# Kernel tuning notes

Measured on AMD Instinct MI355X. Metric: run time of the kernel, lower is better.

Reference implementation:

```python
import jax, jax.numpy as jnp
import numpy as np

B, K, H, W, N = 256, 16, 64, 64, 1024   # batch, channels (n_ch), grid H/W, sampled sites
F_IN = 9 * K - 1                         # 3x3 neighborhood * K channels, minus center channel


def setup_inputs() -> dict:
    key = jax.random.key(0)
    ks = jax.random.split(key, 8)
    z_int = jax.random.randint(ks[0], (B, K, H, W), 0, 16, dtype=jnp.int32)
    bs = jax.random.randint(ks[1], (N,), 0, K, dtype=jnp.int32)
    ii = jax.random.randint(ks[2], (N,), 0, H, dtype=jnp.int32)
    jj = jax.random.randint(ks[3], (N,), 0, W, dtype=jnp.int32)
    W1 = jax.random.normal(ks[4], (F_IN, 128), dtype=jnp.float32) * 0.05
    b1 = jnp.zeros((128,), dtype=jnp.float32)
    W2 = jax.random.normal(ks[5], (128, 16), dtype=jnp.float32) * 0.05
    b2 = jnp.zeros((16,), dtype=jnp.float32)
    return {"z_int": z_int, "bs": bs, "ii": ii, "jj": jj,
            "W1": W1, "b1": b1, "W2": W2, "b2": b2}


def _gather_ctx(z_f, bs, ii, jj):
    # Faithful to get_context ordering: loops di, dj (each in [-1,0,1]) then b,
    # skipping (di==0, dj==0, b==bi). Flattened skip position = 4*K + bi.
    off = jnp.array([-1, 0, 1], dtype=jnp.int32)
    di = jnp.repeat(off, 3)          # [9]
    dj = jnp.tile(off, 3)            # [9]
    ni = (ii[:, None] + di[None, :]) % H   # [N, 9] toroidal wrap
    nj = (jj[:, None] + dj[None, :]) % W   # [N, 9]
    ctx = z_f[:, :, ni, nj]                # [B, K, N, 9]
    ctx = jnp.transpose(ctx, (2, 0, 3, 1)).reshape(N, B, 9 * K)  # [N, B, 9K], (di,dj) major then b
    drop = 4 * K + bs                      # [N] center-channel flat index
    idx = jnp.arange(F_IN, dtype=jnp.int32)
    keep = idx[None, :] + (idx[None, :] >= drop[:, None]).astype(jnp.int32)  # [N, F_IN]
    return jax.vmap(lambda c, k: c[:, k])(ctx, keep)  # [N, B, F_IN]


def reference(z_int, bs, ii, jj, W1, b1, W2, b2):
    z_f = z_int.astype(jnp.float32) / 15.0
    ctx = _gather_ctx(z_f, bs, ii, jj)                 # [N, B, 9K-1]
    h = jax.nn.relu(jnp.einsum('nbf,fh->nbh', ctx, W1) + b1)
    logits = jnp.einsum('nbh,hc->nbc', h, W2) + b2     # [N, B, 16]
    pred = jnp.argmax(logits, axis=-1)                 # [N, B]
    tgt = z_int[:, bs, ii, jj].T                       # [N, B]
    rate = jnp.mean((pred != tgt).astype(jnp.float32)) # np.mean of per-site mean == global mean
    return rate
```

## Files before the change

kernel.cpp:

```cpp
#include <hip/hip_runtime.h>
#include <stdint.h>

#define NB 1024
#define BB 256
#define KK 16
#define HH 64
#define WW 64
#define F_FULL 144
#define HDIM 128
#define CDIM 16
#define KPAD 160
#define APITCH 168
#define HPITCH 136
#define ABYTES (64 * APITCH * 2)
#define HBYTES (64 * HPITCH * 2)
#define NCTR 128

typedef __bf16 bf16x8 __attribute__((ext_vector_type(8)));
typedef float f32x4 __attribute__((ext_vector_type(4)));

#define W1T_OFF 1024
#define W1T_BYTES (16 * HDIM * KPAD * 2)
#define W2B_OFF (W1T_OFF + W1T_BYTES)
#define W2B_BYTES (CDIM * HDIM * 2)
#define ZT_OFF (W2B_OFF + W2B_BYTES)

__device__ __forceinline__ unsigned short bf16_bits(float v) {
    __bf16 b = (__bf16)v;
    return __builtin_bit_cast(unsigned short, b);
}

#define TP 144
__global__ __launch_bounds__(256) void prep_kernel(
    const int* __restrict__ z, const float* __restrict__ W1,
    const float* __restrict__ W2, uint8_t* __restrict__ zt,
    unsigned short* __restrict__ W1t, unsigned short* __restrict__ W2b,
    int* __restrict__ counters) {
    int bid = blockIdx.x;
    int t = threadIdx.x;
    if (bid < 4096) {
        __shared__ uint8_t tile[32 * TP];
        int bx = bid & 127;
        int by = bid >> 7;
        int c0 = bx * 32, r0 = by * 128;
#pragma unroll
        for (int i = 0; i < 4; ++i) {
            int lin = i * 256 + t;
            int c = lin & 31;
            int rq = lin >> 5;
            uchar4 v;
            v.x = (uint8_t)z[(size_t)(r0 + rq * 4 + 0) * 4096 + c0 + c];
            v.y = (uint8_t)z[(size_t)(r0 + rq * 4 + 1) * 4096 + c0 + c];
            v.z = (uint8_t)z[(size_t)(r0 + rq * 4 + 2) * 4096 + c0 + c];
            v.w = (uint8_t)z[(size_t)(r0 + rq * 4 + 3) * 4096 + c0 + c];
            *(uchar4*)(tile + c * TP + rq * 4) = v;
        }
        __syncthreads();
        int cy = t >> 3, rx = t & 7;
        uint4 v = *(const uint4*)(tile + cy * TP + rx * 16);
        *(uint4*)(zt + (size_t)(c0 + cy) * 4096 + r0 + rx * 16) = v;
    } else if (bid < 5376) {
        int idx = (bid - 4096) * 256 + t;
        int k = idx % KPAD;
        int h = (idx / KPAD) % HDIM;
        int s = idx / (KPAD * HDIM);
        int drop = 4 * KK + s;
        float val = 0.0f;
        if (k < F_FULL && k != drop) {
            int src = k - (k > drop ? 1 : 0);
            val = W1[src * HDIM + h];
        }
        W1t[idx] = bf16_bits(val);
    } else {
        int idx = (bid - 5376) * 256 + t;
        if (idx < CDIM * HDIM) {
            int k = idx % HDIM;
            int c = idx / HDIM;
            W2b[idx] = bf16_bits(W2[k * CDIM + c]);
        }
        if (bid == 5376 && t < NCTR) counters[t] = 0;
    }
}

__global__ __launch_bounds__(256, 2) void main_kernel(
    const uint8_t* __restrict__ zt, const unsigned short* __restrict__ W1t,
    const float* __restrict__ b1, const unsigned short* __restrict__ W2b,
    const float* __restrict__ b2, const int* __restrict__ bs,
    const int* __restrict__ ii, const int* __restrict__ jj,
    int* __restrict__ counters) {
    __shared__ __align__(16) unsigned char smem[2 * ABYTES + HBYTES];
    unsigned short* sA0 = (unsigned short*)smem;
    unsigned short* sA1 = (unsigned short*)(smem + ABYTES);
    unsigned short* sH = (unsigned short*)(smem + 2 * ABYTES);

    int t = threadIdx.x;
    int n = blockIdx.x;
    int wave = t >> 6, lane = t & 63;
    int l15 = lane & 15, l4 = lane >> 4;

    int in_ = ii[n], jn = jj[n], sn = bs[n];

    const unsigned short* w1s = W1t + (size_t)sn * (HDIM * KPAD);
    int n0 = wave * 32;
    bf16x8 Bf[2][5];
#pragma unroll
    for (int nt = 0; nt < 2; ++nt)
#pragma unroll
        for (int ks = 0; ks < 5; ++ks)
            Bf[nt][ks] = *(const bf16x8*)(w1s + (n0 + nt * 16 + l15) * KPAD + ks * 32 + l4 * 8);
    bf16x8 Bf2[4];
#pragma unroll
    for (int ks = 0; ks < 4; ++ks)
        Bf2[ks] = *(const bf16x8*)(W2b + l15 * HDIM + ks * 32 + l4 * 8);
    float b1v0 = b1[n0 + l15], b1v1 = b1[n0 + 16 + l15];
    float b2v = b2[l15];

    if (t < 192) {
        int b = t / 3, part = t % 3;
        *(uint4*)(sA0 + b * APITCH + F_FULL + part * 8) = make_uint4(0, 0, 0, 0);
        *(uint4*)(sA1 + b * APITCH + F_FULL + part * 8) = make_uint4(0, 0, 0, 0);
    }

    uint4 g0, g1, g2;
    auto gload = [&](int tile) {
        int b = (t & 63) + tile * 64;
        int p0 = t >> 6;
        int ni0 = (in_ + p0 / 3 - 1) & (HH - 1);
        int nj0 = (jn + p0 % 3 - 1) & (WW - 1);
        g0 = *(const uint4*)(zt + (((size_t)(ni0 * WW + nj0) * BB + b) << 4));
        int p1 = p0 + 4;
        int ni1 = (in_ + p1 / 3 - 1) & (HH - 1);
        int nj1 = (jn + p1 % 3 - 1) & (WW - 1);
        g1 = *(const uint4*)(zt + (((size_t)(ni1 * WW + nj1) * BB + b) << 4));
        if (t < 64) {
            int ni2 = (in_ + 1) & (HH - 1);
            int nj2 = (jn + 1) & (WW - 1);
            g2 = *(const uint4*)(zt + (((size_t)(ni2 * WW + nj2) * BB + b) << 4));
        }
    };
    auto gwrite = [&](unsigned short* dst) {
        int b = t & 63;
        int p0 = t >> 6;
        auto conv = [&](uint4 raw, int p) {
            const uint8_t* bytes = (const uint8_t*)&raw;
            union { __bf16 h[16]; uint4 q[2]; } u;
#pragma unroll
            for (int k = 0; k < 16; ++k)
                u.h[k] = (__bf16)((float)bytes[k] * (1.0f / 15.0f));
            uint4* d = (uint4*)(dst + b * APITCH + p * 16);
            d[0] = u.q[0];
            d[1] = u.q[1];
        };
        conv(g0, p0);
        conv(g1, p0 + 4);
        if (t < 64) conv(g2, 8);
    };

    gload(0);
    gwrite(sA0);
    int err = 0;
    size_t tbase = ((size_t)(in_ * WW + jn) * BB) << 4;

    for (int tile = 0; tile < 4; ++tile) {
        unsigned short* sA = (tile & 1) ? sA1 : sA0;
        unsigned short* sAnext = (tile & 1) ? sA0 : sA1;

        if (tile < 3) gload(tile + 1);
        __syncthreads();

        int bg0 = tile * 64 + wave * 16 + l4 * 4;
        int tv4[4];
#pragma unroll
        for (int r = 0; r < 4; ++r)
            tv4[r] = zt[tbase + ((size_t)(bg0 + r) << 4) + sn];

        f32x4 acc[4][2] = {};
#pragma unroll
        for (int mt = 0; mt < 4; ++mt) {
            bf16x8 Af[5];
#pragma unroll
            for (int ks = 0; ks < 5; ++ks)
                Af[ks] = *(const bf16x8*)(sA + (mt * 16 + l15) * APITCH + ks * 32 + l4 * 8);
#pragma unroll
            for (int ks = 0; ks < 5; ++ks) {
                acc[mt][0] = __builtin_amdgcn_mfma_f32_16x16x32_bf16(Af[ks], Bf[0][ks], acc[mt][0], 0, 0, 0);
                acc[mt][1] = __builtin_amdgcn_mfma_f32_16x16x32_bf16(Af[ks], Bf[1][ks], acc[mt][1], 0, 0, 0);
            }
        }

#pragma unroll
        for (int mt = 0; mt < 4; ++mt)
#pragma unroll
            for (int nt = 0; nt < 2; ++nt) {
                float bv = nt ? b1v1 : b1v0;
                int hcol = n0 + nt * 16 + l15;
#pragma unroll
                for (int r = 0; r < 4; ++r) {
                    int b = mt * 16 + l4 * 4 + r;
                    float v = fmaxf(acc[mt][nt][r] + bv, 0.0f);
                    sH[b * HPITCH + hcol] = bf16_bits(v);
                }
            }
        __syncthreads();

        f32x4 acc2 = {};
#pragma unroll
        for (int ks = 0; ks < 4; ++ks) {
            bf16x8 Af = *(const bf16x8*)(sH + (wave * 16 + l15) * HPITCH + ks * 32 + l4 * 8);
            acc2 = __builtin_amdgcn_mfma_f32_16x16x32_bf16(Af, Bf2[ks], acc2, 0, 0, 0);
        }

#pragma unroll
        for (int r = 0; r < 4; ++r) {
            float v = acc2[r] + b2v;
            int idx = l15;
#pragma unroll
            for (int m = 1; m < 16; m <<= 1) {
                float ov = __shfl_xor(v, m);
                int oi = __shfl_xor(idx, m);
                if (ov > v || (ov == v && oi < idx)) { v = ov; idx = oi; }
            }
            unsigned long long mm = __ballot(l15 == 0 && idx != tv4[r]);
            err += (int)__popcll(mm);
        }

        if (tile < 3) gwrite(sAnext);
    }

    if (lane == 0) atomicAdd(&counters[n & (NCTR - 1)], err);
}

__global__ void finalize_kernel(const int* __restrict__ counters, float* __restrict__ out) {
    int t = threadIdx.x;
    int s = counters[t] + counters[t + 64];
#pragma unroll
    for (int m = 32; m; m >>= 1) s += __shfl_down(s, m);
    if (t == 0) out[0] = (float)s / (float)(NB * BB);
}

extern "C" void kernel_launch(void* const* d_in, const int* in_sizes, int n_in,
                              void* d_out, int out_size, void* d_ws, size_t ws_size,
                              hipStream_t stream) {
    const int* z = (const int*)d_in[0];
    const int* bs = (const int*)d_in[1];
    const int* ii = (const int*)d_in[2];
    const int* jj = (const int*)d_in[3];
    const float* W1 = (const float*)d_in[4];
    const float* b1 = (const float*)d_in[5];
    const float* W2 = (const float*)d_in[6];
    const float* b2 = (const float*)d_in[7];
    float* out = (float*)d_out;

    uint8_t* ws = (uint8_t*)d_ws;
    int* counters = (int*)ws;
    unsigned short* W1t = (unsigned short*)(ws + W1T_OFF);
    unsigned short* W2b = (unsigned short*)(ws + W2B_OFF);
    uint8_t* zt = ws + ZT_OFF;

    prep_kernel<<<5384, 256, 0, stream>>>(z, W1, W2, zt, W1t, W2b, counters);
    main_kernel<<<NB, 256, 0, stream>>>(zt, W1t, b1, W2b, b2, bs, ii, jj, counters);
    finalize_kernel<<<1, 64, 0, stream>>>(counters, out);
}
```

Baseline: 144.6 us.

## Software-pipeline layer-1 and layer-2 stages with double-buffered hidden tile

Restructures the per-tile loop into a five-stage software pipeline. Layer-2 MFMA and argmax for the previous tile run in the same step as the layer-1 MFMA for the current tile, with the hidden activations double-buffered in shared memory. This drops one __syncthreads per tile, and global loads are now issued two tiles ahead. The cost is extra LDS per block, which may reduce occupancy, and longer register live ranges.

```diff
diff --git a/kernel.cpp b/kernel.cpp
--- a/kernel.cpp
+++ b/kernel.cpp
@@ -88,10 +88,11 @@
     const float* __restrict__ b2, const int* __restrict__ bs,
     const int* __restrict__ ii, const int* __restrict__ jj,
     int* __restrict__ counters) {
-    __shared__ __align__(16) unsigned char smem[2 * ABYTES + HBYTES];
+    __shared__ __align__(16) unsigned char smem[2 * ABYTES + 2 * HBYTES];
     unsigned short* sA0 = (unsigned short*)smem;
     unsigned short* sA1 = (unsigned short*)(smem + ABYTES);
-    unsigned short* sH = (unsigned short*)(smem + 2 * ABYTES);
+    unsigned short* sH0 = (unsigned short*)(smem + 2 * ABYTES);
+    unsigned short* sH1 = (unsigned short*)(smem + 2 * ABYTES + HBYTES);
 
     int t = threadIdx.x;
     int n = blockIdx.x;
@@ -122,9 +123,9 @@
     }
 
     uint4 g0, g1, g2;
+    int p0 = t >> 6;
     auto gload = [&](int tile) {
         int b = (t & 63) + tile * 64;
-        int p0 = t >> 6;
         int ni0 = (in_ + p0 / 3 - 1) & (HH - 1);
         int nj0 = (jn + p0 % 3 - 1) & (WW - 1);
         g0 = *(const uint4*)(zt + (((size_t)(ni0 * WW + nj0) * BB + b) << 4));
@@ -140,7 +141,6 @@
     };
     auto gwrite = [&](unsigned short* dst) {
         int b = t & 63;
-        int p0 = t >> 6;
         auto conv = [&](uint4 raw, int p) {
             const uint8_t* bytes = (const uint8_t*)&raw;
             union { __bf16 h[16]; uint4 q[2]; } u;
@@ -158,73 +158,83 @@
 
     gload(0);
     gwrite(sA0);
+    gload(1);
+
     int err = 0;
     size_t tbase = ((size_t)(in_ * WW + jn) * BB) << 4;
 
-    for (int tile = 0; tile < 4; ++tile) {
-        unsigned short* sA = (tile & 1) ? sA1 : sA0;
-        unsigned short* sAnext = (tile & 1) ? sA0 : sA1;
-
-        if (tile < 3) gload(tile + 1);
+    for (int s = 0; s < 5; ++s) {
         __syncthreads();
 
-        int bg0 = tile * 64 + wave * 16 + l4 * 4;
         int tv4[4];
-#pragma unroll
-        for (int r = 0; r < 4; ++r)
-            tv4[r] = zt[tbase + ((size_t)(bg0 + r) << 4) + sn];
+        if (s >= 1) {
+            int bg0 = (s - 1) * 64 + wave * 16 + l4 * 4;
+#pragma unroll
+            for (int r = 0; r < 4; ++r)
+                tv4[r] = zt[tbase + ((size_t)(bg0 + r) << 4) + sn];
+        }
 
         f32x4 acc[4][2] = {};
-#pragma unroll
-        for (int mt = 0; mt < 4; ++mt) {
-            bf16x8 Af[5];
-#pragma unroll
-            for (int ks = 0; ks < 5; ++ks)
-                Af[ks] = *(const bf16x8*)(sA + (mt * 16 + l15) * APITCH + ks * 32 + l4 * 8);
-#pragma unroll
-            for (int ks = 0; ks < 5; ++ks) {
-                acc[mt][0] = __builtin_amdgcn_mfma_f32_16x16x32_bf16(Af[ks], Bf[0][ks], acc[mt][0], 0, 0, 0);
-                acc[mt][1] = __builtin_amdgcn_mfma_f32_16x16x32_bf16(Af[ks], Bf[1][ks], acc[mt][1], 0, 0, 0);
-            }
-        }
-
-#pragma unroll
-        for (int mt = 0; mt < 4; ++mt)
-#pragma unroll
-            for (int nt = 0; nt < 2; ++nt) {
-                float bv = nt ? b1v1 : b1v0;
-                int hcol = n0 + nt * 16 + l15;
-#pragma unroll
-                for (int r = 0; r < 4; ++r) {
-                    int b = mt * 16 + l4 * 4 + r;
-                    float v = fmaxf(acc[mt][nt][r] + bv, 0.0f);
-                    sH[b * HPITCH + hcol] = bf16_bits(v);
+        if (s < 4) {
+            const unsigned short* sA = (s & 1) ? sA1 : sA0;
+#pragma unroll
+            for (int mt = 0; mt < 4; ++mt) {
+                bf16x8 Af[5];
+#pragma unroll
+                for (int ks = 0; ks < 5; ++ks)
+                    Af[ks] = *(const bf16x8*)(sA + (mt * 16 + l15) * APITCH + ks * 32 + l4 * 8);
+#pragma unroll
+                for (int ks = 0; ks < 5; ++ks) {
+                    acc[mt][0] = __builtin_amdgcn_mfma_f32_16x16x32_bf16(Af[ks], Bf[0][ks], acc[mt][0], 0, 0, 0);
+                    acc[mt][1] = __builtin_amdgcn_mfma_f32_16x16x32_bf16(Af[ks], Bf[1][ks], acc[mt][1], 0, 0, 0);
                 }
             }
-        __syncthreads();
-
-        f32x4 acc2 = {};
-#pragma unroll
-        for (int ks = 0; ks < 4; ++ks) {
-            bf16x8 Af = *(const bf16x8*)(sH + (wave * 16 + l15) * HPITCH + ks * 32 + l4 * 8);
-            acc2 = __builtin_amdgcn_mfma_f32_16x16x32_bf16(Af, Bf2[ks], acc2, 0, 0, 0);
-        }
-
-#pragma unroll
-        for (int r = 0; r < 4; ++r) {
-            float v = acc2[r] + b2v;
-            int idx = l15;
-#pragma unroll
-            for (int m = 1; m < 16; m <<= 1) {
-                float ov = __shfl_xor(v, m);
-                int oi = __shfl_xor(idx, m);
-                if (ov > v || (ov == v && oi < idx)) { v = ov; idx = oi; }
+        }
+
+        if (s >= 1) {
+            const unsigned short* sHp = ((s - 1) & 1) ? sH1 : sH0;
+            f32x4 acc2 = {};
+#pragma unroll
+            for (int ks = 0; ks < 4; ++ks) {
+                bf16x8 Af = *(const bf16x8*)(sHp + (wave * 16 + l15) * HPITCH + ks * 32 + l4 * 8);
+                acc2 = __builtin_amdgcn_mfma_f32_16x16x32_bf16(Af, Bf2[ks], acc2, 0, 0, 0);
             }
-            unsigned long long mm = __ballot(l15 == 0 && idx != tv4[r]);
-            err += (int)__popcll(mm);
-        }
-
-        if (tile < 3) gwrite(sAnext);
+#pragma unroll
+            for (int r = 0; r < 4; ++r) {
+                float v = acc2[r] + b2v;
+                int idx = l15;
+#pragma unroll
+                for (int m = 1; m < 16; m <<= 1) {
+                    float ov = __shfl_xor(v, m);
+                    int oi = __shfl_xor(idx, m);
+                    if (ov > v || (ov == v && oi < idx)) { v = ov; idx = oi; }
+                }
+                unsigned long long mm = __ballot(l15 == 0 && idx != tv4[r]);
+                err += (int)__popcll(mm);
+            }
+        }
+
+        if (s < 4) {
+            unsigned short* sHc = (s & 1) ? sH1 : sH0;
+#pragma unroll
+            for (int mt = 0; mt < 4; ++mt)
+#pragma unroll
+                for (int nt = 0; nt < 2; ++nt) {
+                    float bv = nt ? b1v1 : b1v0;
+                    int hcol = n0 + nt * 16 + l15;
+#pragma unroll
+                    for (int r = 0; r < 4; ++r) {
+                        int b = mt * 16 + l4 * 4 + r;
+                        float v = fmaxf(acc[mt][nt][r] + bv, 0.0f);
+                        sHc[b * HPITCH + hcol] = bf16_bits(v);
+                    }
+                }
+        }
+
+        if (s < 3) {
+            gwrite((s & 1) ? sA0 : sA1);
+            if (s < 2) gload(s + 2);
+        }
     }
 
     if (lane == 0) atomicAdd(&counters[n & (NCTR - 1)], err);
```

Result: no change. 145.1 us (+0.3%).
